# Optimization experiments

Measured on AMD Instinct MI355X. Metric: run time of the kernel, lower is better.

The kernel has to match this reference:

```python
import jax, jax.numpy as jnp
import numpy as np

D = 1024          # d_model
DI = 2 * D        # d_inner (expand=2)
N = 16            # d_state
R = 64            # dt_rank
K = 4             # d_conv
B_, S = 2, 2048


def setup_inputs() -> dict:
    key = jax.random.key(0)
    ks = jax.random.split(key, 16)
    sc = 0.02
    inp = {
        "x": jax.random.normal(ks[0], (B_, S, D), jnp.float32),
        "c": jax.random.normal(ks[1], (B_, 2 * D), jnp.float32),
        "w": jax.random.normal(ks[2], (B_, S, D), jnp.float32),
        # LayerNorm
        "ln_w": jnp.ones((D,), jnp.float32),
        "ln_b": jnp.zeros((D,), jnp.float32),
        # adaLN: Linear(2D -> 3D)
        "ada_w": jax.random.normal(ks[3], (3 * D, 2 * D), jnp.float32) * sc,
        "ada_b": jnp.zeros((3 * D,), jnp.float32),
        # Mamba params
        "in_proj_w": jax.random.normal(ks[4], (2 * DI, D), jnp.float32) * sc,
        "conv_w": jax.random.normal(ks[5], (DI, K), jnp.float32) * sc,
        "conv_b": jnp.zeros((DI,), jnp.float32),
        "x_proj_w": jax.random.normal(ks[6], (R + 2 * N, DI), jnp.float32) * sc,
        "dt_proj_w": jax.random.normal(ks[7], (DI, R), jnp.float32) * sc,
        "dt_proj_b": jnp.zeros((DI,), jnp.float32),
        "A_log": jnp.log(jnp.broadcast_to(jnp.arange(1, N + 1, dtype=jnp.float32), (DI, N))),
        "D_skip": jnp.ones((DI,), jnp.float32),
        "out_proj_w": jax.random.normal(ks[8], (D, DI), jnp.float32) * sc,
    }
    return inp


def _mamba(u, in_proj_w, conv_w, conv_b, x_proj_w, dt_proj_w, dt_proj_b, A_log, D_skip, out_proj_w):
    b, s, d = u.shape
    xz = jnp.einsum('bsd,ed->bse', u, in_proj_w)          # [b,s,2*DI]
    xc, z = jnp.split(xz, 2, axis=-1)                     # each [b,s,DI]
    # causal depthwise conv1d, kernel K
    xp = jnp.pad(xc, ((0, 0), (K - 1, 0), (0, 0)))
    xc = sum(xp[:, k:k + s, :] * conv_w[:, k] for k in range(K)) + conv_b
    xc = jax.nn.silu(xc)
    x_dbl = jnp.einsum('bsd,ed->bse', xc, x_proj_w)       # [b,s,R+2N]
    dt, Bmat, Cmat = jnp.split(x_dbl, [R, R + N], axis=-1)
    delta = jax.nn.softplus(jnp.einsum('bsr,dr->bsd', dt, dt_proj_w) + dt_proj_b)  # [b,s,DI]
    A = -jnp.exp(A_log)                                    # [DI,N]

    def step(h, t):
        dlt, Bt, Ct, ut = t                                # [b,DI],[b,N],[b,N],[b,DI]
        dA = jnp.exp(dlt[:, :, None] * A)                  # [b,DI,N]
        h = dA * h + (dlt * ut)[:, :, None] * Bt[:, None, :]
        y = jnp.einsum('bdn,bn->bd', h, Ct)
        return h, y

    h0 = jnp.zeros((b, DI, N), xc.dtype)
    xs = (delta.transpose(1, 0, 2), Bmat.transpose(1, 0, 2), Cmat.transpose(1, 0, 2), xc.transpose(1, 0, 2))
    _, ys = jax.lax.scan(step, h0, xs)                     # ys [s,b,DI]
    y = ys.transpose(1, 0, 2) + xc * D_skip
    y = y * jax.nn.silu(z)
    return jnp.einsum('bsd,ed->bse', y, out_proj_w)        # [b,s,D]


def reference(x, c, w, ln_w, ln_b, ada_w, ada_b, in_proj_w, conv_w, conv_b,
              x_proj_w, dt_proj_w, dt_proj_b, A_log, D_skip, out_proj_w):
    # adaLN: SiLU -> Linear -> chunk into shift/scale/gate
    mod = jnp.einsum('bc,ec->be', jax.nn.silu(c), ada_w) + ada_b
    shift, scale, gate = jnp.split(mod, 3, axis=-1)        # each [b,D]
    # LayerNorm over last dim
    mu = jnp.mean(x, axis=-1, keepdims=True)
    var = jnp.mean(jnp.square(x - mu), axis=-1, keepdims=True)
    xn = (x - mu) * jax.lax.rsqrt(var + 1e-5) * ln_w + ln_b
    # modulate
    xs = xn * (1.0 + scale[:, None, :]) + shift[:, None, :]
    y = _mamba(xs, in_proj_w, conv_w, conv_b, x_proj_w, dt_proj_w, dt_proj_b, A_log, D_skip, out_proj_w)
    return x + gate[:, None, :] * y
```

## Files before the change

### kernel.cpp

```cpp
#include <hip/hip_runtime.h>
#include <hip/hip_bf16.h>
#include <math.h>

#define D_MODEL 1024
#define DIN     2048
#define NST     16
#define RDT     64
#define KC      4
#define BB      2
#define SS      2048
#define NTOK    (BB*SS)
#define NCH     32
#define CL      (SS/NCH)
#define NQT     (BB*NCH*DIN)
#define QOFF    ((size_t)NQT*NST)
#define LOG2E   1.4426950408889634f

typedef short short8 __attribute__((ext_vector_type(8)));
typedef float floatx4 __attribute__((ext_vector_type(4)));

__device__ __forceinline__ float silu_f(float v) { return v / (1.f + __expf(-v)); }
__device__ __forceinline__ float softplus_f(float v) {
    return fmaxf(v, 0.f) + __logf(1.f + __expf(-fabsf(v)));
}
__device__ __forceinline__ unsigned short f2bf(float f) {
    __hip_bfloat16 h = __float2bfloat16(f);
    unsigned short u; __builtin_memcpy(&u, &h, 2); return u;
}
__device__ __forceinline__ float bf2f(unsigned short u) {
    __hip_bfloat16 h; __builtin_memcpy(&h, &u, 2); return __bfloat162float(h);
}
__device__ __forceinline__ void gload16(const void* g, void* l) {
    __builtin_amdgcn_global_load_lds(
        (const __attribute__((address_space(1))) void*)g,
        (__attribute__((address_space(3))) void*)l, 16, 0, 0);
}

#define C3N1 (2*DIN*D_MODEL)
#define C3N2 (96*DIN)
#define C3N3 (D_MODEL*DIN)
#define NCAST ((C3N1 + C3N2 + C3N3) / 1024)
__global__ void k_cast3(const float* __restrict__ s1, unsigned short* __restrict__ d1,
                        const float* __restrict__ s2, unsigned short* __restrict__ d2,
                        const float* __restrict__ s3, unsigned short* __restrict__ d3,
                        const float* __restrict__ c, const float* __restrict__ ada_w,
                        const float* __restrict__ ada_b, float* __restrict__ mod) {
    if (blockIdx.x < NCAST) {
        int i = (blockIdx.x * 256 + threadIdx.x) * 4;
        const float* s; unsigned short* d;
        if (i < C3N1)              { s = s1 + i;               d = d1 + i; }
        else if (i < C3N1 + C3N2)  { s = s2 + (i - C3N1);      d = d2 + (i - C3N1); }
        else                       { s = s3 + (i - C3N1 - C3N2); d = d3 + (i - C3N1 - C3N2); }
        float4 v = *(const float4*)s;
        ushort4 o;
        o.x = f2bf(v.x); o.y = f2bf(v.y); o.z = f2bf(v.z); o.w = f2bf(v.w);
        *(ushort4*)d = o;
    } else {
        int bid2 = blockIdx.x - NCAST;
        int wid  = bid2 * 4 + (threadIdx.x >> 6);
        int lane = threadIdx.x & 63;
        if (wid >= BB * 3 * D_MODEL) return;
        int b = wid / (3 * D_MODEL);
        int e = wid % (3 * D_MODEL);
        const float* crow = c + (size_t)b * 2 * D_MODEL;
        const float* wrow = ada_w + (size_t)e * 2 * D_MODEL;
        float acc = 0.f;
        for (int j = lane; j < 2 * D_MODEL; j += 64)
            acc += silu_f(crow[j]) * wrow[j];
        for (int off = 32; off > 0; off >>= 1) acc += __shfl_down(acc, off, 64);
        if (lane == 0) mod[(size_t)b * 3 * D_MODEL + e] = acc + ada_b[e];
    }
}

__global__ void k_lnmod(const float* __restrict__ x, const float* __restrict__ ln_w,
                        const float* __restrict__ ln_b, const float* __restrict__ mod,
                        unsigned short* __restrict__ xs) {
    int tok = blockIdx.x;
    int b   = tok / SS;
    const float* xrow = x + (size_t)tok * D_MODEL;
    float xv[4];
    float s1 = 0.f, s2 = 0.f;
    #pragma unroll
    for (int r = 0; r < 4; r++) {
        float v = xrow[threadIdx.x + r * 256];
        xv[r] = v; s1 += v; s2 += v * v;
    }
    __shared__ float red1[4], red2[4];
    for (int off = 32; off > 0; off >>= 1) {
        s1 += __shfl_down(s1, off, 64);
        s2 += __shfl_down(s2, off, 64);
    }
    int wid = threadIdx.x >> 6, lane = threadIdx.x & 63;
    if (lane == 0) { red1[wid] = s1; red2[wid] = s2; }
    __syncthreads();
    s1 = red1[0] + red1[1] + red1[2] + red1[3];
    s2 = red2[0] + red2[1] + red2[2] + red2[3];
    float mu   = s1 / D_MODEL;
    float var  = s2 / D_MODEL - mu * mu;
    float rstd = rsqrtf(var + 1e-5f);
    const float* shiftp = mod + (size_t)b * 3 * D_MODEL;
    const float* scalep = shiftp + D_MODEL;
    unsigned short* orow = xs + (size_t)tok * D_MODEL;
    #pragma unroll
    for (int r = 0; r < 4; r++) {
        int i = threadIdx.x + r * 256;
        float v = (xv[r] - mu) * rstd * ln_w[i] + ln_b[i];
        orow[i] = f2bf(v * (1.f + scalep[i]) + shiftp[i]);
    }
}

template <int MODE>
__global__ void k_mfma2(const unsigned short* __restrict__ A,
                        const unsigned short* __restrict__ W,
                        void* __restrict__ Cv, int ldc, int K) {
    constexpr int TM = 128, TN = 128;
    __shared__ char smem[(TM + TN) * 64 * 2];
    short* lA = (short*)smem;
    short* lB = (short*)(smem + TM * 64 * 2);

    int t    = threadIdx.x;
    int lane = t & 63;
    int w    = t >> 6;
    int quad = lane >> 4, l15 = lane & 15;
    int wm   = (w & 1) * 64, wn = (w >> 1) * 64;
    int nbx = gridDim.x;
    int lin = blockIdx.y * nbx + blockIdx.x;
    int cpx = (nbx * gridDim.y) >> 3;
    int swz = (lin & 7) * cpx + (lin >> 3);
    int row0 = (swz / nbx) * TM;
    int col0 = (swz % nbx) * TN;
    int kbase = (MODE == 1) ? blockIdx.z * 256 : (MODE == 5) ? blockIdx.z * 1024 : 0;
    int kiters = (MODE == 1) ? 256 : (MODE == 5) ? 1024 : K;

    const unsigned short* pa[4]; int la_[4];
    #pragma unroll
    for (int p = 0; p < 4; p++) {
        int s = t + p * 256;
        int row = s >> 3;
        int kc  = (s & 7) ^ (row & 7);
        pa[p] = A + (size_t)(row0 + row) * K + kbase + kc * 8;
        la_[p] = s * 8;
    }
    const unsigned short* pb[4]; int lb_[4];
    #pragma unroll
    for (int p = 0; p < 4; p++) {
        int s = t + p * 256;
        int row = s >> 3;
        int kc  = (s & 7) ^ (row & 7);
        int grow = col0 + row;
        if (MODE == 1) grow = grow < 95 ? grow : 95;
        pb[p] = W + (size_t)grow * K + kbase + kc * 8;
        lb_[p] = s * 8;
    }

    const short8* A8 = (const short8*)lA;
    const short8* B8 = (const short8*)lB;
    int sw = l15 & 7;
    floatx4 acc[4][4] = {};

    for (int k0 = 0; k0 < kiters; k0 += 64) {
        #pragma unroll
        for (int p = 0; p < 4; p++) gload16(pa[p] + k0, lA + la_[p]);
        #pragma unroll
        for (int p = 0; p < 4; p++) gload16(pb[p] + k0, lB + lb_[p]);
        __builtin_amdgcn_s_waitcnt(0);
        __syncthreads();
        #pragma unroll
        for (int kc = 0; kc < 2; kc++) {
            int koff = (kc * 4 + quad) ^ sw;
            short8 af[4], bfr[4];
            #pragma unroll
            for (int i = 0; i < 4; i++) af[i]  = A8[(wm + i * 16 + l15) * 8 + koff];
            #pragma unroll
            for (int j = 0; j < 4; j++) bfr[j] = B8[(wn + j * 16 + l15) * 8 + koff];
            #pragma unroll
            for (int i = 0; i < 4; i++)
                #pragma unroll
                for (int j = 0; j < 4; j++)
                    acc[i][j] = __builtin_amdgcn_mfma_f32_16x16x32_bf16(
                        af[i], bfr[j], acc[i][j], 0, 0, 0);
        }
        __syncthreads();
    }

    if constexpr (MODE == 0 || MODE == 5) {
        unsigned short* Cc = (unsigned short*)Cv;
        if constexpr (MODE == 5) Cc += (size_t)blockIdx.z * NTOK * D_MODEL;
        short* st = (short*)smem;
        #pragma unroll
        for (int half = 0; half < 2; half++) {
            __syncthreads();
            if ((w & 1) == half) {
                #pragma unroll
                for (int i = 0; i < 4; i++)
                    #pragma unroll
                    for (int j = 0; j < 4; j++)
                        #pragma unroll
                        for (int rg = 0; rg < 4; rg++)
                            st[(i * 16 + quad * 4 + rg) * 136 + wn + j * 16 + l15] =
                                (short)f2bf(acc[i][j][rg]);
            }
            __syncthreads();
            #pragma unroll
            for (int p = 0; p < 4; p++) {
                int idx = p * 256 + t;
                int r = idx >> 4, sx = idx & 15;
                *(short8*)(Cc + (size_t)(row0 + half * 64 + r) * ldc + col0 + sx * 8) =
                    *(const short8*)(st + r * 136 + sx * 8);
            }
        }
    } else {
        float* Cz = (float*)Cv + (size_t)blockIdx.z * NTOK * 96;
        #pragma unroll
        for (int i = 0; i < 4; i++)
            #pragma unroll
            for (int j = 0; j < 4; j++) {
                int cc = col0 + wn + j * 16 + l15;
                if (cc < 96) {
                    #pragma unroll
                    for (int rg = 0; rg < 4; rg++)
                        Cz[(size_t)(row0 + wm + i * 16 + quad * 4 + rg) * 96 + cc] =
                            acc[i][j][rg];
                }
            }
    }
}

__global__ void k_red8(const float* __restrict__ part, float* __restrict__ x_dbl) {
    int i = (blockIdx.x * 256 + threadIdx.x) * 4;
    const size_t SZ = (size_t)NTOK * 96;
    float4 s = *(const float4*)(part + i);
    #pragma unroll
    for (int z = 1; z < 8; z++) {
        float4 a = *(const float4*)(part + z * SZ + i);
        s.x += a.x; s.y += a.y; s.z += a.z; s.w += a.w;
    }
    *(float4*)(x_dbl + i) = s;
}

__global__ void k_redout(const unsigned short* __restrict__ part, const float* __restrict__ x,
                         const float* __restrict__ mod, float* __restrict__ out) {
    int i = (blockIdx.x * 256 + threadIdx.x) * 4;
    const size_t SZ = (size_t)NTOK * D_MODEL;
    float sx_ = 0.f, sy = 0.f, sz = 0.f, sw = 0.f;
    #pragma unroll
    for (int z = 0; z < 2; z++) {
        ushort4 a = *(const ushort4*)(part + z * SZ + i);
        sx_ += bf2f(a.x); sy += bf2f(a.y); sz += bf2f(a.z); sw += bf2f(a.w);
    }
    int e  = i & (D_MODEL - 1);
    int bb = i >> 21;
    float4 xv = *(const float4*)(x + i);
    float4 g  = *(const float4*)(mod + (size_t)bb * 3 * D_MODEL + 2 * D_MODEL + e);
    float4 o;
    o.x = xv.x + g.x * sx_; o.y = xv.y + g.y * sy;
    o.z = xv.z + g.z * sz;  o.w = xv.w + g.w * sw;
    *(float4*)(out + i) = o;
}

__global__ void k_dtproj(const float* __restrict__ A,
                         const float* __restrict__ W,
                         unsigned short* __restrict__ C,
                         const float* __restrict__ bias) {
    __shared__ float As[16][68];
    __shared__ float Ws[16][68];
    int t = threadIdx.x;
    int row0 = blockIdx.y * 64;
    int col0 = blockIdx.x * 64;
    int lr = t >> 2;
    int lk = (t & 3) * 4;
    int ty = t >> 4, tx = t & 15;
    float acc[4][4] = {};
    for (int k0 = 0; k0 < RDT; k0 += 16) {
        const float* ap = A + (size_t)(row0 + lr) * 96 + k0 + lk;
        float a0 = ap[0], a1 = ap[1], a2 = ap[2], a3 = ap[3];
        const float* wp = W + (size_t)(col0 + lr) * RDT + k0 + lk;
        float b0 = wp[0], b1 = wp[1], b2 = wp[2], b3 = wp[3];
        __syncthreads();
        As[lk + 0][lr] = a0; As[lk + 1][lr] = a1; As[lk + 2][lr] = a2; As[lk + 3][lr] = a3;
        Ws[lk + 0][lr] = b0; Ws[lk + 1][lr] = b1; Ws[lk + 2][lr] = b2; Ws[lk + 3][lr] = b3;
        __syncthreads();
        #pragma unroll
        for (int kk = 0; kk < 16; kk++) {
            float av[4], bv[4];
            #pragma unroll
            for (int i = 0; i < 4; i++) av[i] = As[kk][ty * 4 + i];
            #pragma unroll
            for (int j = 0; j < 4; j++) bv[j] = Ws[kk][tx * 4 + j];
            #pragma unroll
            for (int i = 0; i < 4; i++)
                #pragma unroll
                for (int j = 0; j < 4; j++)
                    acc[i][j] += av[i] * bv[j];
        }
    }
    int cc = col0 + tx * 4;
    float b0 = bias[cc], b1 = bias[cc + 1], b2 = bias[cc + 2], b3 = bias[cc + 3];
    #pragma unroll
    for (int i = 0; i < 4; i++) {
        int r = row0 + ty * 4 + i;
        ushort4 o;
        o.x = f2bf(softplus_f(acc[i][0] + b0));
        o.y = f2bf(softplus_f(acc[i][1] + b1));
        o.z = f2bf(softplus_f(acc[i][2] + b2));
        o.w = f2bf(softplus_f(acc[i][3] + b3));
        *(ushort4*)(C + (size_t)r * DIN + cc) = o;
    }
}

__global__ void k_conv(const unsigned short* __restrict__ xz, const float* __restrict__ conv_w,
                       const float* __restrict__ conv_b, unsigned short* __restrict__ xc) {
    int idx = blockIdx.x * 256 + threadIdx.x;
    int d8  = (idx & (DIN / 8 - 1)) * 8;
    int tok = idx >> 8;
    int s   = tok & (SS - 1);
    int b   = tok >> 11;
    float acc[8];
    float4 cb0 = *(const float4*)(conv_b + d8);
    float4 cb1 = *(const float4*)(conv_b + d8 + 4);
    acc[0] = cb0.x; acc[1] = cb0.y; acc[2] = cb0.z; acc[3] = cb0.w;
    acc[4] = cb1.x; acc[5] = cb1.y; acc[6] = cb1.z; acc[7] = cb1.w;
    float wv[8][KC];
    #pragma unroll
    for (int j = 0; j < 8; j++) {
        float4 w4 = *(const float4*)(conv_w + (d8 + j) * KC);
        wv[j][0] = w4.x; wv[j][1] = w4.y; wv[j][2] = w4.z; wv[j][3] = w4.w;
    }
    #pragma unroll
    for (int k = 0; k < KC; k++) {
        int ss = s - (KC - 1) + k;
        if (ss >= 0) {
            short8 v = *(const short8*)(xz + (size_t)(b * SS + ss) * (2 * DIN) + d8);
            #pragma unroll
            for (int j = 0; j < 8; j++)
                acc[j] += bf2f((unsigned short)v[j]) * wv[j][k];
        }
    }
    short8 o;
    #pragma unroll
    for (int j = 0; j < 8; j++) o[j] = (short)f2bf(silu_f(acc[j]));
    *(short8*)(xc + (size_t)tok * DIN + d8) = o;
}

__global__ void k_scan1(const unsigned short* __restrict__ delta,
                        const unsigned short* __restrict__ xc, const float* __restrict__ x_dbl,
                        float* __restrict__ PQ) {
    __shared__ float bS[CL][NST];
    int idx = blockIdx.x * 256 + threadIdx.x;
    int d = idx & (DIN - 1);
    int c = (idx / DIN) % NCH;
    int b = idx / (NCH * DIN);
    int tok0 = b * SS + c * CL;
    for (int f = threadIdx.x; f < CL * NST; f += 256) {
        int s = f >> 4, n = f & 15;
        bS[s][n] = x_dbl[(size_t)(tok0 + s) * 96 + RDT + n];
    }
    float q[NST];
    #pragma unroll
    for (int n = 0; n < NST; n++) q[n] = 0.f;
    __syncthreads();
    size_t base = (size_t)tok0 * DIN + d;
    float sdlt = 0.f;
    unsigned short pd[4], pu[4];
    #pragma unroll
    for (int j = 0; j < 4; j++) { pd[j] = delta[base + j * DIN]; pu[j] = xc[base + j * DIN]; }
    for (int g = 0; g < CL / 4; g++) {
        unsigned short cd[4], cu[4];
        #pragma unroll
        for (int j = 0; j < 4; j++) { cd[j] = pd[j]; cu[j] = pu[j]; }
        if (g + 1 < CL / 4) {
            size_t nb = base + (size_t)(g * 4 + 4) * DIN;
            #pragma unroll
            for (int j = 0; j < 4; j++) { pd[j] = delta[nb + j * DIN]; pu[j] = xc[nb + j * DIN]; }
        }
        #pragma unroll
        for (int js = 0; js < 4; js++) {
            int s = g * 4 + js;
            float dlt = bf2f(cd[js]);
            float du  = dlt * bf2f(cu[js]);
            sdlt += dlt;
            float r = __expf(-dlt);
            float p = 1.f;
            #pragma unroll
            for (int n = 0; n < NST; n++) {
                p *= r;
                q[n] = p * q[n] + du * bS[s][n];
            }
        }
    }
    PQ[idx] = sdlt;
    float* qp = PQ + QOFF + (size_t)idx * 4;
    #pragma unroll
    for (int n4 = 0; n4 < 4; n4++)
        *(float4*)(qp + (size_t)n4 * NQT * 4) =
            make_float4(q[4*n4], q[4*n4+1], q[4*n4+2], q[4*n4+3]);
}

__global__ void k_scan2(float* __restrict__ PQ) {
    int idx = blockIdx.x * 256 + threadIdx.x;
    int n = idx & (NST - 1);
    int d = (idx >> 4) & (DIN - 1);
    int b = idx >> 15;
    float A2n = -(float)(n + 1) * LOG2E;
    const size_t cq = (size_t)DIN * 4;
    const size_t cd = DIN;
    size_t qbase = QOFF + ((size_t)(n >> 2) * NQT + (size_t)b * NCH * DIN + d) * 4 + (n & 3);
    size_t sbase = (size_t)b * NCH * DIN + d;
    float h = 0.f;
    float sv[4], qv[4];
    #pragma unroll
    for (int j = 0; j < 4; j++) {
        sv[j] = PQ[sbase + j * cd];
        qv[j] = PQ[qbase + j * cq];
    }
    for (int g = 0; g < NCH / 4; g++) {
        float cs_[4], cq_[4];
        #pragma unroll
        for (int j = 0; j < 4; j++) { cs_[j] = sv[j]; cq_[j] = qv[j]; }
        if (g + 1 < NCH / 4) {
            size_t nbs = sbase + (size_t)(g * 4 + 4) * cd;
            size_t nbq = qbase + (size_t)(g * 4 + 4) * cq;
            #pragma unroll
            for (int j = 0; j < 4; j++) {
                sv[j] = PQ[nbs + j * cd];
                qv[j] = PQ[nbq + j * cq];
            }
        }
        #pragma unroll
        for (int j = 0; j < 4; j++) {
            PQ[qbase + (size_t)(g * 4 + j) * cq] = h;
            h = exp2f(A2n * cs_[j]) * h + cq_[j];
        }
    }
}

__global__ void k_scan3(const unsigned short* __restrict__ delta,
                        const unsigned short* __restrict__ xc, const unsigned short* __restrict__ xz,
                        const float* __restrict__ x_dbl,
                        const float* __restrict__ D_skip, const float* __restrict__ PQ,
                        unsigned short* __restrict__ y_bf) {
    __shared__ float bcS[CL][2 * NST];
    int idx = blockIdx.x * 256 + threadIdx.x;
    int d = idx & (DIN - 1);
    int c = (idx / DIN) % NCH;
    int b = idx / (NCH * DIN);
    int tok0 = b * SS + c * CL;
    for (int f = threadIdx.x; f < CL * 2 * NST; f += 256) {
        int s = f >> 5, j = f & 31;
        bcS[s][j] = x_dbl[(size_t)(tok0 + s) * 96 + RDT + j];
    }
    float h[NST];
    const float* hp = PQ + QOFF + (size_t)idx * 4;
    #pragma unroll
    for (int n4 = 0; n4 < 4; n4++) {
        float4 v = *(const float4*)(hp + (size_t)n4 * NQT * 4);
        h[4*n4] = v.x; h[4*n4+1] = v.y; h[4*n4+2] = v.z; h[4*n4+3] = v.w;
    }
    float Dv = D_skip[d];
    __syncthreads();
    size_t base  = (size_t)tok0 * DIN + d;
    size_t zbase = (size_t)tok0 * 2 * DIN + DIN + d;
    unsigned short pd[4], pu[4], pz[4];
    #pragma unroll
    for (int j = 0; j < 4; j++) {
        pd[j] = delta[base + j * DIN];
        pu[j] = xc[base + j * DIN];
        pz[j] = xz[zbase + (size_t)j * 2 * DIN];
    }
    for (int g = 0; g < CL / 4; g++) {
        unsigned short cd[4], cu[4], cz[4];
        #pragma unroll
        for (int j = 0; j < 4; j++) { cd[j] = pd[j]; cu[j] = pu[j]; cz[j] = pz[j]; }
        if (g + 1 < CL / 4) {
            size_t nb = base + (size_t)(g * 4 + 4) * DIN;
            size_t nz = zbase + (size_t)(g * 4 + 4) * 2 * DIN;
            #pragma unroll
            for (int j = 0; j < 4; j++) {
                pd[j] = delta[nb + j * DIN];
                pu[j] = xc[nb + j * DIN];
                pz[j] = xz[nz + (size_t)j * 2 * DIN];
            }
        }
        #pragma unroll
        for (int js = 0; js < 4; js++) {
            int s = g * 4 + js;
            float dlt = bf2f(cd[js]);
            float u   = bf2f(cu[js]);
            float du  = dlt * u;
            float r = __expf(-dlt);
            float p = 1.f;
            float y = 0.f;
            #pragma unroll
            for (int n = 0; n < NST; n++) {
                p *= r;
                h[n] = p * h[n] + du * bcS[s][n];
                y += h[n] * bcS[s][NST + n];
            }
            float z = bf2f(cz[js]);
            y_bf[base + (size_t)s * DIN] = f2bf((y + u * Dv) * silu_f(z));
        }
    }
}

extern "C" void kernel_launch(void* const* d_in, const int* in_sizes, int n_in,
                              void* d_out, int out_size, void* d_ws, size_t ws_size,
                              hipStream_t stream) {
    const float* x         = (const float*)d_in[0];
    const float* c         = (const float*)d_in[1];
    const float* ln_w      = (const float*)d_in[3];
    const float* ln_b      = (const float*)d_in[4];
    const float* ada_w     = (const float*)d_in[5];
    const float* ada_b     = (const float*)d_in[6];
    const float* in_proj_w = (const float*)d_in[7];
    const float* conv_w    = (const float*)d_in[8];
    const float* conv_b    = (const float*)d_in[9];
    const float* x_proj_w  = (const float*)d_in[10];
    const float* dt_proj_w = (const float*)d_in[11];
    const float* dt_proj_b = (const float*)d_in[12];
    const float* D_skip    = (const float*)d_in[14];
    const float* out_proj_w= (const float*)d_in[15];
    float* out = (float*)d_out;

    float* ws = (float*)d_ws;
    size_t off = 0;
    float* mod              = ws + off; off += (size_t)BB * 3 * D_MODEL;
    unsigned short* xs_bf   = (unsigned short*)(ws + off); off += (size_t)NTOK * D_MODEL / 2;
    unsigned short* xz_bf   = (unsigned short*)(ws + off); off += (size_t)NTOK * 2 * DIN / 2;
    unsigned short* xc_bf   = (unsigned short*)(ws + off); off += (size_t)NTOK * DIN / 2;
    float* x_dbl            = ws + off; off += (size_t)NTOK * 96;
    unsigned short* delta_bf= (unsigned short*)(ws + off); off += (size_t)NTOK * DIN / 2;
    unsigned short* y_bf    = (unsigned short*)(ws + off); off += (size_t)NTOK * DIN / 2;
    unsigned short* w_xp_bf = (unsigned short*)(ws + off); off += (size_t)96 * DIN / 2;
    unsigned short* w_out_bf= (unsigned short*)(ws + off); off += (size_t)D_MODEL * DIN / 2;
    float* pool             = ws + off; off += 4 * QOFF;
    unsigned short* w_in_bf  = (unsigned short*)pool;
    float* xp_part           = pool;
    float* PQ                = pool;
    unsigned short* op_part  = (unsigned short*)pool;

    k_cast3<<<dim3(NCAST + (BB * 3 * D_MODEL) / 4), dim3(256), 0, stream>>>(
        in_proj_w, w_in_bf, x_proj_w, w_xp_bf, out_proj_w, w_out_bf,
        c, ada_w, ada_b, mod);
    k_lnmod<<<dim3(NTOK), dim3(256), 0, stream>>>(x, ln_w, ln_b, mod, xs_bf);
    k_mfma2<0><<<dim3((2 * DIN) / 128, NTOK / 128), dim3(256), 0, stream>>>(
        xs_bf, w_in_bf, xz_bf, 2 * DIN, D_MODEL);
    k_conv<<<dim3((NTOK * DIN) / (8 * 256)), dim3(256), 0, stream>>>(xz_bf, conv_w, conv_b, xc_bf);
    k_mfma2<1><<<dim3(1, NTOK / 128, 8), dim3(256), 0, stream>>>(
        xc_bf, w_xp_bf, xp_part, 96, DIN);
    k_red8<<<dim3((NTOK * 96) / 1024), dim3(256), 0, stream>>>(xp_part, x_dbl);
    k_dtproj<<<dim3(DIN / 64, NTOK / 64), dim3(256), 0, stream>>>(
        x_dbl, dt_proj_w, delta_bf, dt_proj_b);
    k_scan1<<<dim3((BB * NCH * DIN) / 256), dim3(256), 0, stream>>>(
        delta_bf, xc_bf, x_dbl, PQ);
    k_scan2<<<dim3((BB * DIN * NST) / 256), dim3(256), 0, stream>>>(PQ);
    k_scan3<<<dim3((BB * NCH * DIN) / 256), dim3(256), 0, stream>>>(
        delta_bf, xc_bf, xz_bf, x_dbl, D_skip, PQ, y_bf);
    k_mfma2<5><<<dim3(D_MODEL / 128, NTOK / 128, 2), dim3(256), 0, stream>>>(
        y_bf, w_out_bf, op_part, D_MODEL, DIN);
    k_redout<<<dim3((NTOK * D_MODEL) / 1024), dim3(256), 0, stream>>>(op_part, x, mod, out);
}
```

Measured before the change: 357.0 us.

## Add 256x256 double-buffered MFMA GEMM for in_proj and double scan chunks

Replaces the 128x128 k_mfma2 MODE 0 in_proj GEMM with a dedicated 512-thread kernel using 256x256 tiles, double-buffered LDS with async global loads, swizzled LDS layout and s_setprio around MFMA bursts. The aim is more operand reuse per tile and overlap of loads with compute in the largest GEMM. Separately, the scan chunk count is doubled (NCH 32 to 64), which shortens each sequential chunk and exposes more parallelism in the scan kernels at the cost of a larger carry buffer. The pool sizing is also changed, and the block swizzle is removed from k_mfma2.

Result: faster. 348.8 us (-2.3%).

```diff
diff --git a/kernel.cpp b/kernel.cpp
--- a/kernel.cpp
+++ b/kernel.cpp
@@ -10,7 +10,7 @@
 #define BB      2
 #define SS      2048
 #define NTOK    (BB*SS)
-#define NCH     32
+#define NCH     64
 #define CL      (SS/NCH)
 #define NQT     (BB*NCH*DIN)
 #define QOFF    ((size_t)NQT*NST)
@@ -109,6 +109,112 @@
     }
 }
 
+__global__ __launch_bounds__(512, 1)
+void k_mfma256(const unsigned short* __restrict__ A,
+               const unsigned short* __restrict__ W,
+               unsigned short* __restrict__ C) {
+    __shared__ char smem[65536];
+    constexpr int K = D_MODEL, ldc = 2 * DIN, NT = K / 32;
+    int t    = threadIdx.x;
+    int lane = t & 63;
+    int w    = t >> 6;
+    int quad = lane >> 4, l15 = lane & 15;
+    int wm   = (w >> 2) * 128, wn = (w & 3) * 64;
+    int row0 = blockIdx.y * 256, col0 = blockIdx.x * 256;
+
+    const unsigned short* pa[2]; const unsigned short* pb[2]; int lso[2];
+    #pragma unroll
+    for (int p = 0; p < 2; p++) {
+        int s = t + p * 512;
+        int r = s >> 2, cc = s & 3;
+        int g = cc ^ ((r >> 1) & 3);
+        pa[p] = A + (size_t)(row0 + r) * K + g * 8;
+        pb[p] = W + (size_t)(col0 + r) * K + g * 8;
+        lso[p] = s * 16;
+    }
+    int koff = quad ^ ((l15 >> 1) & 3);
+
+    floatx4 acc[8][4] = {};
+
+    auto issue = [&](int kt, int c) {
+        char* base = smem + c * 32768;
+        #pragma unroll
+        for (int p = 0; p < 2; p++) gload16(pa[p] + kt * 32, base + lso[p]);
+        #pragma unroll
+        for (int p = 0; p < 2; p++) gload16(pb[p] + kt * 32, base + 16384 + lso[p]);
+    };
+
+    issue(0, 0);
+    issue(1, 1);
+    asm volatile("s_waitcnt vmcnt(4)" ::: "memory");
+    __builtin_amdgcn_s_barrier();
+
+    int c = 0;
+    for (int kt = 0; kt < NT; kt++) {
+        const short8* A8 = (const short8*)(smem + c * 32768);
+        const short8* B8 = (const short8*)(smem + c * 32768 + 16384);
+        short8 bq[4];
+        #pragma unroll
+        for (int j = 0; j < 4; j++) bq[j] = B8[(wn + j * 16 + l15) * 4 + koff];
+        #pragma unroll
+        for (int ph = 0; ph < 3; ph++) {
+            short8 a0 = A8[(wm + (2 * ph + 0) * 16 + l15) * 4 + koff];
+            short8 a1 = A8[(wm + (2 * ph + 1) * 16 + l15) * 4 + koff];
+            __builtin_amdgcn_s_setprio(1);
+            #pragma unroll
+            for (int j = 0; j < 4; j++)
+                acc[2 * ph][j] = __builtin_amdgcn_mfma_f32_16x16x32_bf16(a0, bq[j], acc[2 * ph][j], 0, 0, 0);
+            #pragma unroll
+            for (int j = 0; j < 4; j++)
+                acc[2 * ph + 1][j] = __builtin_amdgcn_mfma_f32_16x16x32_bf16(a1, bq[j], acc[2 * ph + 1][j], 0, 0, 0);
+            __builtin_amdgcn_s_setprio(0);
+            __builtin_amdgcn_s_barrier();
+        }
+        short8 a6 = A8[(wm + 6 * 16 + l15) * 4 + koff];
+        short8 a7 = A8[(wm + 7 * 16 + l15) * 4 + koff];
+        asm volatile("s_waitcnt lgkmcnt(0)" ::: "memory");
+        __builtin_amdgcn_sched_barrier(0);
+        __builtin_amdgcn_s_barrier();
+        if (kt + 2 < NT) issue(kt + 2, c);
+        __builtin_amdgcn_s_setprio(1);
+        #pragma unroll
+        for (int j = 0; j < 4; j++)
+            acc[6][j] = __builtin_amdgcn_mfma_f32_16x16x32_bf16(a6, bq[j], acc[6][j], 0, 0, 0);
+        #pragma unroll
+        for (int j = 0; j < 4; j++)
+            acc[7][j] = __builtin_amdgcn_mfma_f32_16x16x32_bf16(a7, bq[j], acc[7][j], 0, 0, 0);
+        __builtin_amdgcn_s_setprio(0);
+        if (kt + 2 < NT)      { asm volatile("s_waitcnt vmcnt(4)" ::: "memory"); }
+        else if (kt + 1 < NT) { asm volatile("s_waitcnt vmcnt(0)" ::: "memory"); }
+        __builtin_amdgcn_s_barrier();
+        c ^= 1;
+    }
+
+    short* st = (short*)smem;
+    for (int qq = 0; qq < 4; qq++) {
+        __syncthreads();
+        if ((w >> 2) == (qq >> 1)) {
+            int ib = (qq & 1) * 4;
+            #pragma unroll
+            for (int i2 = 0; i2 < 4; i2++)
+                #pragma unroll
+                for (int j = 0; j < 4; j++)
+                    #pragma unroll
+                    for (int rg = 0; rg < 4; rg++)
+                        st[(i2 * 16 + quad * 4 + rg) * 264 + wn + j * 16 + l15] =
+                            (short)f2bf(acc[ib + i2][j][rg]);
+        }
+        __syncthreads();
+        #pragma unroll
+        for (int p = 0; p < 4; p++) {
+            int idx = p * 512 + t;
+            int r = idx >> 5, ch = idx & 31;
+            *(short8*)(C + (size_t)(row0 + qq * 64 + r) * ldc + col0 + ch * 8) =
+                *(const short8*)(st + r * 264 + ch * 8);
+        }
+    }
+}
+
 template <int MODE>
 __global__ void k_mfma2(const unsigned short* __restrict__ A,
                         const unsigned short* __restrict__ W,
@@ -123,14 +229,10 @@
     int w    = t >> 6;
     int quad = lane >> 4, l15 = lane & 15;
     int wm   = (w & 1) * 64, wn = (w >> 1) * 64;
-    int nbx = gridDim.x;
-    int lin = blockIdx.y * nbx + blockIdx.x;
-    int cpx = (nbx * gridDim.y) >> 3;
-    int swz = (lin & 7) * cpx + (lin >> 3);
-    int row0 = (swz / nbx) * TM;
-    int col0 = (swz % nbx) * TN;
-    int kbase = (MODE == 1) ? blockIdx.z * 256 : (MODE == 5) ? blockIdx.z * 1024 : 0;
-    int kiters = (MODE == 1) ? 256 : (MODE == 5) ? 1024 : K;
+    int row0 = blockIdx.y * TM;
+    int col0 = blockIdx.x * TN;
+    int kbase = (MODE == 1) ? blockIdx.z * 256 : blockIdx.z * 1024;
+    int kiters = (MODE == 1) ? 256 : 1024;
 
     const unsigned short* pa[4]; int la_[4];
     #pragma unroll
@@ -183,9 +285,9 @@
         __syncthreads();
     }
 
-    if constexpr (MODE == 0 || MODE == 5) {
+    if constexpr (MODE == 5) {
         unsigned short* Cc = (unsigned short*)Cv;
-        if constexpr (MODE == 5) Cc += (size_t)blockIdx.z * NTOK * D_MODEL;
+        Cc += (size_t)blockIdx.z * NTOK * D_MODEL;
         short* st = (short*)smem;
         #pragma unroll
         for (int half = 0; half < 2; half++) {
@@ -532,7 +634,7 @@
     unsigned short* y_bf    = (unsigned short*)(ws + off); off += (size_t)NTOK * DIN / 2;
     unsigned short* w_xp_bf = (unsigned short*)(ws + off); off += (size_t)96 * DIN / 2;
     unsigned short* w_out_bf= (unsigned short*)(ws + off); off += (size_t)D_MODEL * DIN / 2;
-    float* pool             = ws + off; off += 4 * QOFF;
+    float* pool             = ws + off; off += 2 * QOFF;
     unsigned short* w_in_bf  = (unsigned short*)pool;
     float* xp_part           = pool;
     float* PQ                = pool;
@@ -542,8 +644,8 @@
         in_proj_w, w_in_bf, x_proj_w, w_xp_bf, out_proj_w, w_out_bf,
         c, ada_w, ada_b, mod);
     k_lnmod<<<dim3(NTOK), dim3(256), 0, stream>>>(x, ln_w, ln_b, mod, xs_bf);
-    k_mfma2<0><<<dim3((2 * DIN) / 128, NTOK / 128), dim3(256), 0, stream>>>(
-        xs_bf, w_in_bf, xz_bf, 2 * DIN, D_MODEL);
+    k_mfma256<<<dim3((2 * DIN) / 256, NTOK / 256), dim3(512), 0, stream>>>(
+        xs_bf, w_in_bf, xz_bf);
     k_conv<<<dim3((NTOK * DIN) / (8 * 256)), dim3(256), 0, stream>>>(xz_bf, conv_w, conv_b, xc_bf);
     k_mfma2<1><<<dim3(1, NTOK / 128, 8), dim3(256), 0, stream>>>(
         xc_bf, w_xp_bf, xp_part, 96, DIN);
```
